# Optimization experiments

Hardware: AMD Instinct MI355X
Metric: run time of the kernel (lower is better)

Reference implementation:

```python
import jax, jax.numpy as jnp
import numpy as np

B, C, F, H, W = 8, 16, 256, 112, 112   # batch, cells/image, channels, height, width
NB = 3                                  # tgt_shape = (3, 3) adaptive pool bins


def setup_inputs() -> dict:
    key = jax.random.key(0)
    kf, ky, kx, kry, krx, kn = jax.random.split(key, 6)
    feature_maps = jax.random.normal(kf, (B, F, H, W), jnp.float32)
    N = B * C
    # random rectangular cell blobs with bernoulli interior holes + guaranteed core
    cy = jax.random.randint(ky, (N, 1, 1), 20, H - 20)
    cx = jax.random.randint(kx, (N, 1, 1), 20, W - 20)
    ry = jax.random.randint(kry, (N, 1, 1), 5, 18)
    rx = jax.random.randint(krx, (N, 1, 1), 5, 18)
    yy = jnp.arange(H)[None, :, None]
    xx = jnp.arange(W)[None, None, :]
    rect = (jnp.abs(yy - cy) <= ry) & (jnp.abs(xx - cx) <= rx)
    noise = jax.random.bernoulli(kn, 0.8, (N, H, W))
    core = (jnp.abs(yy - cy) <= 2) & (jnp.abs(xx - cx) <= 2)
    cell_masks = rect & (noise | core)            # [N, H, W] bool, each nonempty
    cell_counts = jnp.full((B,), C, jnp.int32)    # fixed cells per image
    return {"feature_maps": feature_maps, "cell_masks": cell_masks,
            "cell_counts": cell_counts}


def _bin_membership(lo, hi, length):
    # adaptive-pool bin i covers [lo + floor(i*sz/NB), lo + ceil((i+1)*sz/NB))
    i = jnp.arange(NB)
    sz = (hi - lo)[..., None]                      # [B, C, 1]
    start = lo[..., None] + (i * sz) // NB         # [B, C, NB]
    end = lo[..., None] + ((i + 1) * sz + NB - 1) // NB
    pos = jnp.arange(length)
    return (pos >= start[..., None]) & (pos < end[..., None])  # [B, C, NB, L]


def reference(feature_maps, cell_masks, cell_counts):
    Bv, Fv, Hv, Wv = feature_maps.shape
    Cv = cell_masks.shape[0] // Bv
    masks = cell_masks.reshape(Bv, Cv, Hv, Wv)
    # tight bbox per cell (first/last True row and column, exclusive end)
    rows = masks.any(-1)                            # [B, C, H]
    cols = masks.any(-2)                            # [B, C, W]
    y0 = jnp.argmax(rows, -1)
    y1 = Hv - jnp.argmax(rows[..., ::-1], -1)
    x0 = jnp.argmax(cols, -1)
    x1 = Wv - jnp.argmax(cols[..., ::-1], -1)
    ymem = _bin_membership(y0, y1, Hv)              # [B, C, NB, H]
    xmem = _bin_membership(x0, x1, Wv)              # [B, C, NB, W]
    neg = jnp.finfo(feature_maps.dtype).min
    feat = feature_maps[:, None]                    # [B, 1, F, H, W]
    m = masks[:, :, None]                           # [B, C, 1, H, W]
    pooled = []
    for i in range(NB):
        ym = ymem[:, :, i][:, :, None, :, None]     # [B, C, 1, H, 1]
        for j in range(NB):
            xm = xmem[:, :, j][:, :, None, None, :]  # [B, C, 1, 1, W]
            inbin = ym & xm
            # inside bin & mask -> feature; inside bin & ~mask -> 0 (zeroed crop);
            # outside bin -> -inf (excluded from max)
            v = jnp.where(inbin & m, feat, jnp.where(inbin, 0.0, neg))
            pooled.append(v.max((-1, -2)))          # [B, C, F]
    out = jnp.stack(pooled, -1)                     # [B, C, F, 9], index = i*NB + j
    # matches torch pooled.view(-1): flatten order f*9 + i*3 + j
    return out.reshape(Bv * Cv, Fv * NB * NB)
```

## Files before the change

kernel.cpp:

```cpp
#include <hip/hip_runtime.h>
#include <float.h>

#define B_  8
#define C_  16
#define N_  (B_*C_)
#define F_  256
#define H_  112
#define W_  112
#define HW_ (H_*W_)
#define NB_ 3

#define FPAR 8
#define WPB  2
#define FPB  (FPAR*WPB)


__global__ __launch_bounds__(256) void bbox_kernel(const int4* __restrict__ mask4,
                                                   int* __restrict__ bb) {
    int n = blockIdx.x, t = threadIdx.x;
    const int4* m = mask4 + (size_t)n * (HW_ / 4);
    int ymin = 1 << 20, ymax = -1, xmin = 1 << 20, xmax = -1;
    for (int i = t; i < HW_ / 4; i += 256) {
        int4 v = m[i];
        int y = i / 28;
        int xb = (i - y * 28) * 4;
        if (v.x | v.y | v.z | v.w) { ymin = min(ymin, y); ymax = max(ymax, y); }
        if (v.x) { xmin = min(xmin, xb);     xmax = max(xmax, xb);     }
        if (v.y) { xmin = min(xmin, xb + 1); xmax = max(xmax, xb + 1); }
        if (v.z) { xmin = min(xmin, xb + 2); xmax = max(xmax, xb + 2); }
        if (v.w) { xmin = min(xmin, xb + 3); xmax = max(xmax, xb + 3); }
    }
    #pragma unroll
    for (int off = 32; off; off >>= 1) {
        ymin = min(ymin, __shfl_xor(ymin, off));
        ymax = max(ymax, __shfl_xor(ymax, off));
        xmin = min(xmin, __shfl_xor(xmin, off));
        xmax = max(xmax, __shfl_xor(xmax, off));
    }
    __shared__ int red[4][4];
    int wave = t >> 6;
    if ((t & 63) == 0) {
        red[wave][0] = ymin; red[wave][1] = ymax;
        red[wave][2] = xmin; red[wave][3] = xmax;
    }
    __syncthreads();
    if (t == 0) {
        for (int w = 1; w < 4; ++w) {
            ymin = min(ymin, red[w][0]); ymax = max(ymax, red[w][1]);
            xmin = min(xmin, red[w][2]); xmax = max(xmax, red[w][3]);
        }
        int y0 = ymin, y1 = ymax + 1, x0 = xmin, x1 = xmax + 1;
        int* o = bb + n * 16;
        o[0] = y0; o[1] = y1; o[2] = x0; o[3] = x1;
        int szy = y1 - y0, szx = x1 - x0;
        for (int i = 0; i < NB_; ++i) {
            o[4+i]  = y0 + (i*szy)/NB_;
            o[7+i]  = y0 + ((i+1)*szy + NB_-1)/NB_;
            o[10+i] = x0 + (i*szx)/NB_;
            o[13+i] = x0 + ((i+1)*szx + NB_-1)/NB_;
        }
    }
}

__global__ __launch_bounds__(128) void pool_kernel(
        const float* __restrict__ feat, const int* __restrict__ mask,
        const int* __restrict__ bb, float* __restrict__ out) {
    int n = blockIdx.x;
    int b = n >> 4;
    const int* o = bb + n * 16;
    int y0 = o[0], x0 = o[2];
    int bw = o[3] - x0;
    int x0a = x0 & ~3;
    int wbw = (x0 - x0a) + bw;

    int lane = threadIdx.x & 63, wave = threadIdx.x >> 6;
    int xq = lane & 15, rg = lane >> 4;
    int bi = min(rg, 2);
    int xq4 = (4 * xq < wbw) ? 4 * xq : 0;
    int f0 = blockIdx.y * FPB + wave * FPAR;
    size_t rowoff = (size_t)y0 * W_ + x0a + xq4;
    const float* gp = feat + (size_t)(b * F_ + f0) * HW_ + rowoff;
    const int*   mp = mask + (size_t)n * HW_ + rowoff;

    int ysb  = o[4 + bi];
    int yeb1 = o[7 + bi] - 1;
    int Tmax = max(o[7] - o[4], max(o[8] - o[5], o[9] - o[6]));

    float acc[4][FPAR];
    #pragma unroll
    for (int s = 0; s < 4; ++s)
        #pragma unroll
        for (int pp = 0; pp < FPAR; ++pp) acc[s][pp] = -FLT_MAX;

    for (int t = 0; t < Tmax; ++t) {
        int off = (min(ysb + t, yeb1) - y0) * W_;
        int4 m4 = *(const int4*)(mp + off);
        float4 c[FPAR];
        #pragma unroll
        for (int pp = 0; pp < FPAR; ++pp)
            c[pp] = *(const float4*)(gp + (size_t)pp * HW_ + off);
        #pragma unroll
        for (int pp = 0; pp < FPAR; ++pp) {
            acc[0][pp] = fmaxf(acc[0][pp], m4.x ? c[pp].x : 0.f);
            acc[1][pp] = fmaxf(acc[1][pp], m4.y ? c[pp].y : 0.f);
            acc[2][pp] = fmaxf(acc[2][pp], m4.z ? c[pp].z : 0.f);
            acc[3][pp] = fmaxf(acc[3][pp], m4.w ? c[pp].w : 0.f);
        }
    }

    int xg = x0a + 4 * xq;
    float lim[3][4];
    #pragma unroll
    for (int j = 0; j < 3; ++j) {
        int xs = o[10 + j], xe = o[13 + j];
        #pragma unroll
        for (int s = 0; s < 4; ++s) {
            int xx = xg + s;
            lim[j][s] = (xx >= xs && xx < xe) ? FLT_MAX : -FLT_MAX;
        }
    }
    #pragma unroll
    for (int pp = 0; pp < FPAR; ++pp) {
        float part[3];
        #pragma unroll
        for (int j = 0; j < 3; ++j) {
            float r = fminf(acc[0][pp], lim[j][0]);
            r = fmaxf(r, fminf(acc[1][pp], lim[j][1]));
            r = fmaxf(r, fminf(acc[2][pp], lim[j][2]));
            r = fmaxf(r, fminf(acc[3][pp], lim[j][3]));
            part[j] = r;
        }
        #pragma unroll
        for (int off = 1; off <= 8; off <<= 1) {
            #pragma unroll
            for (int j = 0; j < 3; ++j)
                part[j] = fmaxf(part[j], __shfl_xor(part[j], off));
        }
        if (xq == 0 && rg < 3) {
            float* op = out + (size_t)(n * F_ + f0 + pp) * 9 + rg * 3;
            op[0] = part[0]; op[1] = part[1]; op[2] = part[2];
        }
    }
}

extern "C" void kernel_launch(void* const* d_in, const int* in_sizes, int n_in,
                              void* d_out, int out_size, void* d_ws, size_t ws_size,
                              hipStream_t stream) {
    const float* feat = (const float*)d_in[0];
    const int*   mask = (const int*)d_in[1];
    int* bb = (int*)d_ws;

    bbox_kernel<<<N_, 256, 0, stream>>>((const int4*)mask, bb);
    dim3 grid(N_, F_ / FPB);
    pool_kernel<<<grid, 128, 0, stream>>>(feat, mask, bb, (float*)d_out);
}
```

Baseline: 191.8 us.

## Pack cell mask rows into bitmasks and unroll pool loop by two rows

The bbox kernel now also writes a 64-bit ballot bitmask per bounding-box row, so the pool kernel reads packed per-thread nibbles instead of loading int4 mask values from global memory on every row. The pool loop is unrolled to process two rows per iteration for more loads in flight. FPAR is halved so twice as many blocks cover the feature dimension. This lowers mask traffic and register pressure and raises parallelism. The cost is redundant bitmask reads per block and a packing step that assumes bins span at most 14 rows and boxes at most 40 rows and 64 columns.

```diff
diff --git a/kernel.cpp b/kernel.cpp
--- a/kernel.cpp
+++ b/kernel.cpp
@@ -10,13 +10,17 @@
 #define HW_ (H_*W_)
 #define NB_ 3
 
-#define FPAR 8
+#define FPAR 4
 #define WPB  2
 #define FPB  (FPAR*WPB)
 
+#define RB_STRIDE 40
+#define NPACK 14
+
 
 __global__ __launch_bounds__(256) void bbox_kernel(const int4* __restrict__ mask4,
-                                                   int* __restrict__ bb) {
+                                                   int* __restrict__ bb,
+                                                   unsigned long long* __restrict__ rowbits) {
     int n = blockIdx.x, t = threadIdx.x;
     const int4* m = mask4 + (size_t)n * (HW_ / 4);
     int ymin = 1 << 20, ymax = -1, xmin = 1 << 20, xmax = -1;
@@ -38,6 +42,7 @@
         xmax = max(xmax, __shfl_xor(xmax, off));
     }
     __shared__ int red[4][4];
+    __shared__ int sb[3];
     int wave = t >> 6;
     if ((t & 63) == 0) {
         red[wave][0] = ymin; red[wave][1] = ymax;
@@ -59,11 +64,24 @@
             o[10+i] = x0 + (i*szx)/NB_;
             o[13+i] = x0 + ((i+1)*szx + NB_-1)/NB_;
         }
+        sb[0] = y0; sb[1] = szy; sb[2] = x0 & ~3;
+    }
+    __syncthreads();
+    {
+        int y0 = sb[0], bh = sb[1], x0a = sb[2];
+        int lane = t & 63;
+        const int* mrow = (const int*)mask4 + (size_t)n * HW_ + x0a + lane;
+        for (int dy = wave; dy < bh; dy += 4) {
+            int v = mrow[(size_t)(y0 + dy) * W_];
+            unsigned long long bits = __ballot(v != 0);
+            if (lane == 0) rowbits[n * RB_STRIDE + dy] = bits;
+        }
     }
 }
 
 __global__ __launch_bounds__(128) void pool_kernel(
-        const float* __restrict__ feat, const int* __restrict__ mask,
+        const float* __restrict__ feat,
+        const unsigned long long* __restrict__ rowbits,
         const int* __restrict__ bb, float* __restrict__ out) {
     int n = blockIdx.x;
     int b = n >> 4;
@@ -78,13 +96,22 @@
     int bi = min(rg, 2);
     int xq4 = (4 * xq < wbw) ? 4 * xq : 0;
     int f0 = blockIdx.y * FPB + wave * FPAR;
-    size_t rowoff = (size_t)y0 * W_ + x0a + xq4;
-    const float* gp = feat + (size_t)(b * F_ + f0) * HW_ + rowoff;
-    const int*   mp = mask + (size_t)n * HW_ + rowoff;
+    const float* gp = feat + (size_t)(b * F_ + f0) * HW_ + (size_t)y0 * W_ + x0a + xq4;
 
     int ysb  = o[4 + bi];
     int yeb1 = o[7 + bi] - 1;
     int Tmax = max(o[7] - o[4], max(o[8] - o[5], o[9] - o[6]));
+
+    unsigned long long mynib = 0;
+    {
+        const unsigned long long* rbp = rowbits + n * RB_STRIDE;
+        #pragma unroll
+        for (int u = 0; u < NPACK; ++u) {
+            int dy = min(ysb + u, yeb1) - y0;
+            unsigned long long row = rbp[dy];
+            mynib |= ((row >> (4 * xq)) & 0xFull) << (4 * u);
+        }
+    }
 
     float acc[4][FPAR];
     #pragma unroll
@@ -92,19 +119,29 @@
         #pragma unroll
         for (int pp = 0; pp < FPAR; ++pp) acc[s][pp] = -FLT_MAX;
 
-    for (int t = 0; t < Tmax; ++t) {
-        int off = (min(ysb + t, yeb1) - y0) * W_;
-        int4 m4 = *(const int4*)(mp + off);
-        float4 c[FPAR];
-        #pragma unroll
-        for (int pp = 0; pp < FPAR; ++pp)
-            c[pp] = *(const float4*)(gp + (size_t)pp * HW_ + off);
+    int T2 = (Tmax + 1) >> 1;
+    for (int t = 0; t < T2; ++t) {
+        int u0 = 2 * t, u1 = 2 * t + 1;
+        int off0 = (min(ysb + u0, yeb1) - y0) * W_;
+        int off1 = (min(ysb + u1, yeb1) - y0) * W_;
+        unsigned int nib0 = (unsigned int)(mynib >> (4 * u0)) & 0xFu;
+        unsigned int nib1 = (unsigned int)(mynib >> (4 * u1)) & 0xFu;
+        float4 c0[FPAR], c1[FPAR];
         #pragma unroll
         for (int pp = 0; pp < FPAR; ++pp) {
-            acc[0][pp] = fmaxf(acc[0][pp], m4.x ? c[pp].x : 0.f);
-            acc[1][pp] = fmaxf(acc[1][pp], m4.y ? c[pp].y : 0.f);
-            acc[2][pp] = fmaxf(acc[2][pp], m4.z ? c[pp].z : 0.f);
-            acc[3][pp] = fmaxf(acc[3][pp], m4.w ? c[pp].w : 0.f);
+            c0[pp] = *(const float4*)(gp + (size_t)pp * HW_ + off0);
+            c1[pp] = *(const float4*)(gp + (size_t)pp * HW_ + off1);
+        }
+        #pragma unroll
+        for (int pp = 0; pp < FPAR; ++pp) {
+            acc[0][pp] = fmaxf(acc[0][pp], (nib0 & 1u) ? c0[pp].x : 0.f);
+            acc[1][pp] = fmaxf(acc[1][pp], (nib0 & 2u) ? c0[pp].y : 0.f);
+            acc[2][pp] = fmaxf(acc[2][pp], (nib0 & 4u) ? c0[pp].z : 0.f);
+            acc[3][pp] = fmaxf(acc[3][pp], (nib0 & 8u) ? c0[pp].w : 0.f);
+            acc[0][pp] = fmaxf(acc[0][pp], (nib1 & 1u) ? c1[pp].x : 0.f);
+            acc[1][pp] = fmaxf(acc[1][pp], (nib1 & 2u) ? c1[pp].y : 0.f);
+            acc[2][pp] = fmaxf(acc[2][pp], (nib1 & 4u) ? c1[pp].z : 0.f);
+            acc[3][pp] = fmaxf(acc[3][pp], (nib1 & 8u) ? c1[pp].w : 0.f);
         }
     }
 
@@ -149,8 +186,9 @@
     const float* feat = (const float*)d_in[0];
     const int*   mask = (const int*)d_in[1];
     int* bb = (int*)d_ws;
+    unsigned long long* rowbits = (unsigned long long*)((char*)d_ws + 8192);
 
-    bbox_kernel<<<N_, 256, 0, stream>>>((const int4*)mask, bb);
+    bbox_kernel<<<N_, 256, 0, stream>>>((const int4*)mask, bb, rowbits);
     dim3 grid(N_, F_ / FPB);
-    pool_kernel<<<grid, 128, 0, stream>>>(feat, mask, bb, (float*)d_out);
+    pool_kernel<<<grid, 128, 0, stream>>>(feat, rowbits, bb, (float*)d_out);
 }
```

After: 179.6 us. 6.4% less time.
